# Kernel optimization log

Hardware: AMD Instinct MI355X
Metric: run time of the kernel (lower is better)

The kernel has to match this reference:

```python
import jax, jax.numpy as jnp
import numpy as np

B, N = 16, 300000          # batch, total anchors per image (all FPN levels concatenated)
PRE, POST = 2000, 1000     # num_pre_nms, num_post_nms
NMS_THR = 0.7
MIN_SIZE = 1e-3            # proposal_min_size
IMG_H, IMG_W = 800.0, 1333.0


def setup_inputs() -> dict:
    key = jax.random.key(0)
    k1, k2, k3, k4, k5, k6 = jax.random.split(key, 6)
    cls = jax.random.normal(k1, (B, N), dtype=jnp.float32)
    reg = jax.random.normal(k2, (B, N, 4), dtype=jnp.float32) * 0.1
    # anchors as valid (cx,cy,w,h)->(x1,y1,x2,y2) boxes inside the image
    cx = jax.random.uniform(k3, (B, N), dtype=jnp.float32, minval=0.0, maxval=IMG_W)
    cy = jax.random.uniform(k4, (B, N), dtype=jnp.float32, minval=0.0, maxval=IMG_H)
    w = jax.random.uniform(k5, (B, N), dtype=jnp.float32, minval=16.0, maxval=256.0)
    h = jax.random.uniform(k6, (B, N), dtype=jnp.float32, minval=16.0, maxval=256.0)
    anchors = jnp.stack([cx - 0.5 * w, cy - 0.5 * h, cx + 0.5 * w, cy + 0.5 * h], axis=-1)
    return {"cls": cls, "reg": reg, "anchors": anchors}


def _decode(anchor, reg):
    aw = anchor[:, 2] - anchor[:, 0]
    ah = anchor[:, 3] - anchor[:, 1]
    acx = anchor[:, 0] + 0.5 * aw
    acy = anchor[:, 1] + 0.5 * ah
    dx, dy, dw, dh = reg[:, 0], reg[:, 1], reg[:, 2], reg[:, 3]
    pcx = dx * aw + acx
    pcy = dy * ah + acy
    pw = jnp.exp(dw) * aw
    ph = jnp.exp(dh) * ah
    return jnp.stack([pcx - 0.5 * pw, pcy - 0.5 * ph, pcx + 0.5 * pw, pcy + 0.5 * ph], axis=-1)


def _iou_matrix(boxes):
    # boxes: [K,4] -> pairwise IoU [K,K]
    area = (boxes[:, 2] - boxes[:, 0]) * (boxes[:, 3] - boxes[:, 1])
    lt = jnp.maximum(boxes[:, None, :2], boxes[None, :, :2])
    rb = jnp.minimum(boxes[:, None, 2:], boxes[None, :, 2:])
    wh = jnp.clip(rb - lt, 0.0)
    inter = wh[..., 0] * wh[..., 1]
    union = area[:, None] + area[None, :] - inter
    return inter / jnp.maximum(union, 1e-8)


def _per_image(score, reg, anchor):
    # topk pre-NMS selection (lax.top_k returns score-descending order)
    top_s, idx = jax.lax.top_k(score, PRE)
    boxes = _decode(anchor[idx], reg[idx].reshape(-1, 4))
    # clip to image bounds
    bounds = jnp.array([IMG_W, IMG_H, IMG_W, IMG_H], dtype=boxes.dtype)
    boxes = jnp.clip(boxes, 0.0, bounds)
    # remove small boxes (mask instead of dynamic removal)
    w = boxes[:, 2] - boxes[:, 0]
    h = boxes[:, 3] - boxes[:, 1]
    valid = (w >= MIN_SIZE) & (h >= MIN_SIZE)
    s = jnp.where(valid, top_s, -jnp.inf)
    order = jnp.argsort(-s)  # score-descending, invalid last
    boxes = boxes[order]
    valid = valid[order]
    # greedy NMS: iterate highest-score-first, suppress later boxes with IoU > thr
    iou = _iou_matrix(boxes)
    rng = jnp.arange(PRE)
    def body(i, keep):
        sup = (iou[i] > NMS_THR) & keep[i]
        return keep & jnp.logical_not(sup & (rng > i))
    keep = jax.lax.fori_loop(0, PRE, body, valid)
    # gather kept boxes (score order preserved), pad with zeros past count
    sel = jnp.argsort(jnp.logical_not(keep), stable=True)[:POST]
    return boxes[sel] * keep[sel][:, None].astype(boxes.dtype)


def reference(cls, reg, anchors):
    # [B, POST, 4] proposals per image (zero-padded where fewer than POST kept)
    return jax.vmap(_per_image)(cls, reg, anchors)
```

## Files before the change

kernel.cpp:

```cpp
#include <hip/hip_runtime.h>

#define NB 16
#define NN 300000
#define PRE 2000
#define POST 1000

typedef unsigned long long ull;

static const size_t OFF_HIST1   = 0;
static const size_t OFF_HIST2   = 65536;
static const size_t OFF_HIST3   = 196608;
static const size_t OFF_CANDCNT = 327680;
static const size_t OFF_EQCNT   = 327936;
static const size_t OFF_BITMAP  = 328192;
static const size_t OFF_B1      = 332288;
static const size_t OFF_NEED1   = 332544;
static const size_t OFF_B2      = 332800;
static const size_t OFF_NEED2   = 333056;
static const size_t OFF_B3      = 333312;
static const size_t OFF_NEED3   = 333568;
static const size_t ZERO_BYTES  = 333824;
static const size_t OFF_CAND    = 333824;
static const size_t OFF_EQBUF   = 464896;
static const size_t OFF_SORTED  = 989184;
static const size_t OFF_NVALID  = 1501184;
static const size_t OFF_MASK    = 1501440;

__device__ __forceinline__ unsigned f2u(float f){
  unsigned b = __float_as_uint(f);
  return (b & 0x80000000u) ? ~b : (b | 0x80000000u);
}

#define H1REP 8
#define H1STRIDE 1025
__global__ void k_hist1(const float* __restrict__ cls, unsigned* __restrict__ hist){
  __shared__ unsigned h[H1REP * H1STRIDE];
  int img = blockIdx.y;
  for (int i = threadIdx.x; i < H1REP * H1STRIDE; i += blockDim.x) h[i] = 0;
  __syncthreads();
  const float* p = cls + (size_t)img * NN;
  int stride = gridDim.x * blockDim.x;
  unsigned rep = (threadIdx.x & (H1REP - 1)) * H1STRIDE;
  for (int i = blockIdx.x * blockDim.x + threadIdx.x; i < NN; i += stride)
    atomicAdd(&h[rep + (f2u(p[i]) >> 22)], 1u);
  __syncthreads();
  unsigned* g = hist + img * 1024;
  for (int i = threadIdx.x; i < 1024; i += blockDim.x){
    unsigned v = 0;
    for (int r = 0; r < H1REP; r++) v += h[r * H1STRIDE + i];
    if (v) atomicAdd(&g[i], v);
  }
}

__global__ void k_scan(const unsigned* __restrict__ hist, int bins,
                       const unsigned* __restrict__ tgt, unsigned K0,
                       unsigned* __restrict__ outBin, unsigned* __restrict__ outNeed){
  int img = blockIdx.x;
  int t = threadIdx.x;
  const unsigned* hh = hist + img * bins;
  unsigned K = tgt ? tgt[img] : K0;
  int per = bins >> 8;
  unsigned s = 0;
  for (int q = 0; q < per; q++) s += hh[bins - 1 - (t * per + q)];
  __shared__ unsigned arr[256];
  arr[t] = s;
  __syncthreads();
  for (int off = 1; off < 256; off <<= 1){
    unsigned v = (t >= off) ? arr[t - off] : 0u;
    __syncthreads();
    arr[t] += v;
    __syncthreads();
  }
  unsigned incl = arr[t], excl = incl - s;
  if (excl < K && K <= incl){
    unsigned c = excl;
    for (int q = 0; q < per; q++){
      int b = bins - 1 - (t * per + q);
      unsigned cnt = hh[b];
      if (c + cnt >= K){ outBin[img] = (unsigned)b; outNeed[img] = K - c; break; }
      c += cnt;
    }
  }
}

__global__ void k_hist2(const float* __restrict__ cls, const unsigned* __restrict__ b1,
                        unsigned* __restrict__ hist){
  int img = blockIdx.y;
  unsigned bb1 = b1[img];
  const float* p = cls + (size_t)img * NN;
  unsigned* g = hist + img * 2048;
  int stride = gridDim.x * blockDim.x;
  for (int i = blockIdx.x * blockDim.x + threadIdx.x; i < NN; i += stride){
    unsigned u = f2u(p[i]);
    if ((u >> 22) == bb1) atomicAdd(&g[(u >> 11) & 0x7FFu], 1u);
  }
}

__global__ void k_hist3(const float* __restrict__ cls, const unsigned* __restrict__ b1,
                        const unsigned* __restrict__ b2, unsigned* __restrict__ hist){
  int img = blockIdx.y;
  unsigned pref = (b1[img] << 11) | b2[img];
  const float* p = cls + (size_t)img * NN;
  unsigned* g = hist + img * 2048;
  int stride = gridDim.x * blockDim.x;
  for (int i = blockIdx.x * blockDim.x + threadIdx.x; i < NN; i += stride){
    unsigned u = f2u(p[i]);
    if ((u >> 11) == pref) atomicAdd(&g[u & 0x7FFu], 1u);
  }
}

__global__ void k_compact(const float* __restrict__ cls, const unsigned* __restrict__ b1,
                          const unsigned* __restrict__ b2, const unsigned* __restrict__ b3,
                          unsigned* __restrict__ cand, unsigned* __restrict__ candCnt,
                          unsigned* __restrict__ eqbuf, unsigned* __restrict__ eqCnt){
  __shared__ unsigned lc[1024];
  __shared__ unsigned le[256];
  __shared__ unsigned lcn, len_, baseC, baseE;
  int img = blockIdx.y;
  if (threadIdx.x == 0){ lcn = 0; len_ = 0; }
  __syncthreads();
  unsigned T = (b1[img] << 22) | (b2[img] << 11) | b3[img];
  const float* p = cls + (size_t)img * NN;
  int stride = gridDim.x * blockDim.x;
  for (int i = blockIdx.x * blockDim.x + threadIdx.x; i < NN; i += stride){
    unsigned u = f2u(p[i]);
    if (u > T){
      unsigned pos = atomicAdd(&lcn, 1u);
      if (pos < 1024u) lc[pos] = (unsigned)i;
      else { unsigned g = atomicAdd(&candCnt[img], 1u); if (g < 2048u) cand[img * 2048 + g] = (unsigned)i; }
    } else if (u == T){
      unsigned pos = atomicAdd(&len_, 1u);
      if (pos < 256u) le[pos] = (unsigned)i;
      else { unsigned g = atomicAdd(&eqCnt[img], 1u); if (g < 8192u) eqbuf[img * 8192 + g] = (unsigned)i; }
    }
  }
  __syncthreads();
  unsigned nc = lcn < 1024u ? lcn : 1024u;
  unsigned ne = len_ < 256u ? len_ : 256u;
  if (threadIdx.x == 0){
    if (nc) baseC = atomicAdd(&candCnt[img], nc);
    if (ne) baseE = atomicAdd(&eqCnt[img], ne);
  }
  __syncthreads();
  for (unsigned t = threadIdx.x; t < nc; t += blockDim.x){
    unsigned g = baseC + t;
    if (g < 2048u) cand[img * 2048 + g] = lc[t];
  }
  for (unsigned t = threadIdx.x; t < ne; t += blockDim.x){
    unsigned g = baseE + t;
    if (g < 8192u) eqbuf[img * 8192 + g] = le[t];
  }
}

__global__ __launch_bounds__(1024) void k_sortd(
    const float* __restrict__ cls, const float* __restrict__ reg,
    const float* __restrict__ anch,
    const unsigned* __restrict__ cand, const unsigned* __restrict__ candCnt,
    const unsigned* __restrict__ eqbuf, const unsigned* __restrict__ eqCnt,
    const unsigned* __restrict__ need3,
    float* __restrict__ sorted, unsigned* __restrict__ nvalid){
  __shared__ ull k[2048];
  __shared__ unsigned short p[2048];
  __shared__ unsigned cidx[2048];
  __shared__ float4 bxs[2048];
  __shared__ unsigned nv;
  int img = blockIdx.x, tid = threadIdx.x;
  unsigned need = need3[img];
  unsigned ec = eqCnt[img]; if (ec > 8192u) ec = 8192u;
  unsigned base = candCnt[img]; if (base > 2048u) base = 2048u;
  const unsigned* eq = eqbuf + img * 8192;
  for (int t = tid; t < 2048; t += 1024)
    cidx[t] = (t < (int)base) ? cand[img * 2048 + t] : 0xFFFFFFFFu;
  if (tid == 0) nv = 0;
  __syncthreads();
  if (need >= ec){
    for (unsigned t = tid; t < ec; t += 1024){
      unsigned g = base + t; if (g < 2048u) cidx[g] = eq[t];
    }
  } else {
    for (unsigned t = tid; t < ec; t += 1024){
      unsigned v = eq[t], r = 0;
      for (unsigned s = 0; s < ec; s++) r += (eq[s] < v) ? 1u : 0u;
      if (r < need && base + r < 2048u) cidx[base + r] = v;
    }
  }
  __syncthreads();
  for (int t = tid; t < 2048; t += 1024){
    unsigned i = cidx[t];
    ull key = 0ull;
    float4 box = make_float4(0.f, 0.f, 0.f, 0.f);
    if (t < PRE && i < NN){
      size_t gi = (size_t)img * NN + i;
      float4 a = ((const float4*)anch)[gi];
      float4 r4 = ((const float4*)reg)[gi];
      float sc = cls[gi];
      float aw = a.z - a.x, ah = a.w - a.y;
      float acx = a.x + 0.5f * aw, acy = a.y + 0.5f * ah;
      float pcx = r4.x * aw + acx, pcy = r4.y * ah + acy;
      float pw = expf(r4.z) * aw, ph = expf(r4.w) * ah;
      float x1 = pcx - 0.5f * pw, y1 = pcy - 0.5f * ph;
      float x2 = pcx + 0.5f * pw, y2 = pcy + 0.5f * ph;
      x1 = fminf(fmaxf(x1, 0.f), 1333.f); x2 = fminf(fmaxf(x2, 0.f), 1333.f);
      y1 = fminf(fmaxf(y1, 0.f), 800.f);  y2 = fminf(fmaxf(y2, 0.f), 800.f);
      bool valid = ((x2 - x1) >= 0.001f) && ((y2 - y1) >= 0.001f);
      unsigned up = valid ? f2u(sc) : 0u;
      key = ((ull)up << 32) | (ull)(0xFFFFFFFFu - i);
      box = make_float4(x1, y1, x2, y2);
    }
    k[t] = key; bxs[t] = box; p[t] = (unsigned short)t;
  }
  __syncthreads();
  for (int kk = 2; kk <= 2048; kk <<= 1){
    for (int j = kk >> 1; j > 0; j >>= 1){
      for (int i = tid; i < 2048; i += 1024){
        int ixj = i ^ j;
        if (ixj > i){
          ull ka = k[i], kb = k[ixj];
          bool up = ((i & kk) == 0);
          if (up ? (ka < kb) : (ka > kb)){
            k[i] = kb; k[ixj] = ka;
            unsigned short t2 = p[i]; p[i] = p[ixj]; p[ixj] = t2;
          }
        }
      }
      __syncthreads();
    }
  }
  unsigned c = 0;
  for (int r = tid; r < PRE; r += 1024){
    ((float4*)sorted)[img * PRE + r] = bxs[p[r]];
    if ((unsigned)(k[r] >> 32) != 0u) c++;
  }
  atomicAdd(&nv, c);
  __syncthreads();
  if (tid == 0) nvalid[img] = nv;
}

__global__ __launch_bounds__(512) void k_mask(const float* __restrict__ sorted,
                                              const unsigned* __restrict__ nvalid,
                                              ull* __restrict__ mask, ull* __restrict__ bitmap){
  __shared__ float4 bx[PRE];
  __shared__ float  ar[PRE];
  __shared__ unsigned rowflag[16];
  int img = blockIdx.y, tid = threadIdx.x;
  if (tid < 16) rowflag[tid] = 0;
  for (int i = tid; i < PRE; i += 512){
    float4 b = ((const float4*)sorted)[img * PRE + i];
    bx[i] = b;
    ar[i] = (b.z - b.x) * (b.w - b.y);
  }
  __syncthreads();
  int row = blockIdx.x * 16 + (tid >> 5);
  int w = tid & 31;
  float4 bi = bx[row];
  float ai = ar[row];
  int qlo = (row >= w) ? (((row - w) >> 5) + 1) : 0;
  int qhi = ((PRE - 1 - w) >> 5) + 1;
  ull m = 0;
  for (int q = qlo; q < qhi; q++){
    int j = (q << 5) + w;
    float4 bj = bx[j];
    float xx1 = fmaxf(bi.x, bj.x), yy1 = fmaxf(bi.y, bj.y);
    float xx2 = fminf(bi.z, bj.z), yy2 = fminf(bi.w, bj.w);
    float ww = fmaxf(xx2 - xx1, 0.f), hh = fmaxf(yy2 - yy1, 0.f);
    float inter = ww * hh;
    float uni = ai + ar[j] - inter;
    if (inter / fmaxf(uni, 1e-8f) > 0.7f) m |= (1ull << q);
  }
  mask[((size_t)(img * PRE + row)) * 32 + w] = m;
  if (m) atomicOr(&rowflag[tid >> 5], 1u);
  __syncthreads();
  if (tid < 16){
    int r = blockIdx.x * 16 + tid;
    if (rowflag[tid] && r < (int)nvalid[img])
      atomicOr(&bitmap[img * 32 + (r >> 6)], 1ull << (r & 63));
  }
}

__global__ __launch_bounds__(256) void k_nms(const ull* __restrict__ mask,
                                             const ull* __restrict__ bitmap,
                                             const unsigned* __restrict__ nvalid,
                                             const float* __restrict__ sorted,
                                             float* __restrict__ out){
  __shared__ unsigned rows[2048];
  __shared__ int mcount;
  __shared__ ull cache[192 * 32];
  __shared__ ull keepP[32];
  __shared__ ull keepLin[32];
  __shared__ unsigned cntArr[32], preArr[32];
  int img = blockIdx.x, tid = threadIdx.x;
  int lane = tid & 63, wave = tid >> 6;
  if (tid == 0){
    int m = 0;
    for (int w0 = 0; w0 < 32; w0++){
      ull bits = bitmap[img * 32 + w0];
      while (bits){
        int b = __ffsll(bits) - 1;
        rows[m++] = (unsigned)(w0 * 64 + b);
        bits &= bits - 1;
      }
    }
    mcount = m;
  }
  __syncthreads();
  int m = mcount;
  ull remv = 0;
  for (int base = 0; base < m; base += 192){
    int cnt = min(192, m - base);
    for (int t = tid; t < cnt * 32; t += 256){
      unsigned rr = rows[base + (t >> 5)];
      cache[t] = mask[((size_t)(img * PRE + rr)) * 32 + (t & 31)];
    }
    __syncthreads();
    if (wave == 0){
      for (int q = 0; q < cnt; q++){
        int i = (int)rows[base + q];
        int wi = i & 31, bi = i >> 5;
        int sup = (lane == wi) && ((remv >> bi) & 1ull);
        if (!__any(sup)){
          if (lane < 32) remv |= cache[(q << 5) + lane];
        }
      }
    }
    __syncthreads();
  }
  int nv = (int)nvalid[img];
  if (wave == 0 && lane < 32){
    int cnt2 = (nv > lane) ? (((nv - 1 - lane) >> 5) + 1) : 0;
    ull vm = (cnt2 >= 64) ? ~0ull : ((1ull << cnt2) - 1ull);
    keepP[lane] = (~remv) & vm;
  }
  __syncthreads();
  if (tid < 32){
    ull lin = 0;
    for (int kk = 0; kk < 64; kk++)
      lin |= ((keepP[kk & 31] >> (2 * tid + (kk >> 5))) & 1ull) << kk;
    keepLin[tid] = lin;
    cntArr[tid] = (unsigned)__popcll(lin);
  }
  __syncthreads();
  if (tid < 32){
    unsigned pre = 0;
    for (int w0 = 0; w0 < tid; w0++) pre += cntArr[w0];
    preArr[tid] = pre;
  }
  __syncthreads();
  for (int i = tid; i < PRE; i += 256){
    int w0 = i >> 6, b = i & 63;
    ull kw = keepLin[w0];
    if ((kw >> b) & 1ull){
      unsigned rank = preArr[w0] + (unsigned)__popcll(kw & ((1ull << b) - 1ull));
      if (rank < POST)
        ((float4*)out)[img * POST + rank] = ((const float4*)sorted)[img * PRE + i];
    }
  }
}

extern "C" void kernel_launch(void* const* d_in, const int* in_sizes, int n_in,
                              void* d_out, int out_size, void* d_ws, size_t ws_size,
                              hipStream_t stream){
  const float* cls  = (const float*)d_in[0];
  const float* reg  = (const float*)d_in[1];
  const float* anch = (const float*)d_in[2];
  float* out = (float*)d_out;
  char* ws = (char*)d_ws;

  unsigned* hist1   = (unsigned*)(ws + OFF_HIST1);
  unsigned* hist2   = (unsigned*)(ws + OFF_HIST2);
  unsigned* hist3   = (unsigned*)(ws + OFF_HIST3);
  unsigned* candCnt = (unsigned*)(ws + OFF_CANDCNT);
  unsigned* eqCnt   = (unsigned*)(ws + OFF_EQCNT);
  ull*      bitmap  = (ull*)     (ws + OFF_BITMAP);
  unsigned* b1      = (unsigned*)(ws + OFF_B1);
  unsigned* need1   = (unsigned*)(ws + OFF_NEED1);
  unsigned* b2      = (unsigned*)(ws + OFF_B2);
  unsigned* need2   = (unsigned*)(ws + OFF_NEED2);
  unsigned* b3      = (unsigned*)(ws + OFF_B3);
  unsigned* need3   = (unsigned*)(ws + OFF_NEED3);
  unsigned* cand    = (unsigned*)(ws + OFF_CAND);
  unsigned* eqbuf   = (unsigned*)(ws + OFF_EQBUF);
  float*    sorted  = (float*)   (ws + OFF_SORTED);
  unsigned* nvalid  = (unsigned*)(ws + OFF_NVALID);
  ull*      mask    = (ull*)     (ws + OFF_MASK);

  hipMemsetAsync(ws, 0, ZERO_BYTES, stream);
  hipMemsetAsync(d_out, 0, (size_t)out_size * sizeof(float), stream);

  k_hist1<<<dim3(64, NB), 256, 0, stream>>>(cls, hist1);
  k_scan <<<NB, 256, 0, stream>>>(hist1, 1024, (const unsigned*)nullptr, 2000u, b1, need1);
  k_hist2<<<dim3(64, NB), 256, 0, stream>>>(cls, b1, hist2);
  k_scan <<<NB, 256, 0, stream>>>(hist2, 2048, need1, 0u, b2, need2);
  k_hist3<<<dim3(64, NB), 256, 0, stream>>>(cls, b1, b2, hist3);
  k_scan <<<NB, 256, 0, stream>>>(hist3, 2048, need2, 0u, b3, need3);
  k_compact<<<dim3(64, NB), 256, 0, stream>>>(cls, b1, b2, b3, cand, candCnt, eqbuf, eqCnt);
  k_sortd<<<NB, 1024, 0, stream>>>(cls, reg, anch, cand, candCnt, eqbuf, eqCnt, need3,
                                   sorted, nvalid);
  k_mask<<<dim3(PRE / 16, NB), 512, 0, stream>>>(sorted, nvalid, mask, bitmap);
  k_nms<<<NB, 256, 0, stream>>>(mask, bitmap, nvalid, sorted, out);
}
```

Baseline: 352.1 us.

## Split per-image sort into finalize, parallel decode, and rank-based scatter kernels

Replaces the single-block-per-image kernel that decoded boxes and ran a shared-memory bitonic sort with three kernels. A small finalize kernel completes the candidate list, a grid-wide decode kernel writes keys and boxes to global scratch and counts valid boxes with ballot plus atomics, and a rank kernel spread over 8 blocks per image computes each element's position by counting larger keys. This spreads the sort work across many more compute units and removes the long chain of barrier-separated bitonic stages. The cost is two extra launches, global round trips for keys and boxes, and quadratic comparison work per image.

```diff
diff --git a/kernel.cpp b/kernel.cpp
--- a/kernel.cpp
+++ b/kernel.cpp
@@ -19,12 +19,14 @@
 static const size_t OFF_NEED2   = 333056;
 static const size_t OFF_B3      = 333312;
 static const size_t OFF_NEED3   = 333568;
-static const size_t ZERO_BYTES  = 333824;
-static const size_t OFF_CAND    = 333824;
-static const size_t OFF_EQBUF   = 464896;
-static const size_t OFF_SORTED  = 989184;
-static const size_t OFF_NVALID  = 1501184;
-static const size_t OFF_MASK    = 1501440;
+static const size_t OFF_NVALID  = 333824;
+static const size_t ZERO_BYTES  = 334080;
+static const size_t OFF_CAND    = 334080;
+static const size_t OFF_EQBUF   = 465152;
+static const size_t OFF_KEYS    = 989440;
+static const size_t OFF_BOXTMP  = 1251584;
+static const size_t OFF_SORTED  = 1775872;
+static const size_t OFF_MASK    = 2287872;
 
 __device__ __forceinline__ unsigned f2u(float f){
   unsigned b = __float_as_uint(f);
@@ -152,52 +154,47 @@
   }
 }
 
-__global__ __launch_bounds__(1024) void k_sortd(
-    const float* __restrict__ cls, const float* __restrict__ reg,
-    const float* __restrict__ anch,
-    const unsigned* __restrict__ cand, const unsigned* __restrict__ candCnt,
-    const unsigned* __restrict__ eqbuf, const unsigned* __restrict__ eqCnt,
-    const unsigned* __restrict__ need3,
-    float* __restrict__ sorted, unsigned* __restrict__ nvalid){
-  __shared__ ull k[2048];
-  __shared__ unsigned short p[2048];
-  __shared__ unsigned cidx[2048];
-  __shared__ float4 bxs[2048];
-  __shared__ unsigned nv;
+__global__ void k_finalize(unsigned* __restrict__ cand, const unsigned* __restrict__ candCnt,
+                           const unsigned* __restrict__ eqbuf, const unsigned* __restrict__ eqCnt,
+                           const unsigned* __restrict__ need3){
   int img = blockIdx.x, tid = threadIdx.x;
   unsigned need = need3[img];
   unsigned ec = eqCnt[img]; if (ec > 8192u) ec = 8192u;
-  unsigned base = candCnt[img]; if (base > 2048u) base = 2048u;
+  unsigned base = candCnt[img];
   const unsigned* eq = eqbuf + img * 8192;
-  for (int t = tid; t < 2048; t += 1024)
-    cidx[t] = (t < (int)base) ? cand[img * 2048 + t] : 0xFFFFFFFFu;
-  if (tid == 0) nv = 0;
-  __syncthreads();
+  unsigned* c = cand + img * 2048;
   if (need >= ec){
-    for (unsigned t = tid; t < ec; t += 1024){
-      unsigned g = base + t; if (g < 2048u) cidx[g] = eq[t];
-    }
-  } else {
-    for (unsigned t = tid; t < ec; t += 1024){
-      unsigned v = eq[t], r = 0;
-      for (unsigned s = 0; s < ec; s++) r += (eq[s] < v) ? 1u : 0u;
-      if (r < need && base + r < 2048u) cidx[base + r] = v;
-    }
-  }
-  __syncthreads();
-  for (int t = tid; t < 2048; t += 1024){
-    unsigned i = cidx[t];
-    ull key = 0ull;
-    float4 box = make_float4(0.f, 0.f, 0.f, 0.f);
-    if (t < PRE && i < NN){
+    for (unsigned t = tid; t < ec; t += 256) if (base + t < 2048u) c[base + t] = eq[t];
+    return;
+  }
+  for (unsigned t = tid; t < ec; t += 256){
+    unsigned v = eq[t], r = 0;
+    for (unsigned s = 0; s < ec; s++) r += (eq[s] < v) ? 1u : 0u;
+    if (r < need && base + r < 2048u) c[base + r] = v;
+  }
+}
+
+__global__ void k_decode(const float* __restrict__ cls, const float* __restrict__ reg,
+                         const float* __restrict__ anch, const unsigned* __restrict__ cand,
+                         float* __restrict__ boxTmp, ull* __restrict__ keys,
+                         unsigned* __restrict__ nvalid){
+  int s = blockIdx.x * blockDim.x + threadIdx.x;
+  if (s >= NB * 2048) return;
+  int img = s >> 11, slot = s & 2047;
+  ull key = 0ull;
+  float4 box = make_float4(0.f, 0.f, 0.f, 0.f);
+  bool counted = false;
+  if (slot < PRE){
+    unsigned i = cand[img * 2048 + slot];
+    if (i < NN){
       size_t gi = (size_t)img * NN + i;
       float4 a = ((const float4*)anch)[gi];
-      float4 r4 = ((const float4*)reg)[gi];
+      float4 r = ((const float4*)reg)[gi];
       float sc = cls[gi];
       float aw = a.z - a.x, ah = a.w - a.y;
       float acx = a.x + 0.5f * aw, acy = a.y + 0.5f * ah;
-      float pcx = r4.x * aw + acx, pcy = r4.y * ah + acy;
-      float pw = expf(r4.z) * aw, ph = expf(r4.w) * ah;
+      float pcx = r.x * aw + acx, pcy = r.y * ah + acy;
+      float pw = expf(r.z) * aw, ph = expf(r.w) * ah;
       float x1 = pcx - 0.5f * pw, y1 = pcy - 0.5f * ph;
       float x2 = pcx + 0.5f * pw, y2 = pcy + 0.5f * ph;
       x1 = fminf(fmaxf(x1, 0.f), 1333.f); x2 = fminf(fmaxf(x2, 0.f), 1333.f);
@@ -206,34 +203,30 @@
       unsigned up = valid ? f2u(sc) : 0u;
       key = ((ull)up << 32) | (ull)(0xFFFFFFFFu - i);
       box = make_float4(x1, y1, x2, y2);
-    }
-    k[t] = key; bxs[t] = box; p[t] = (unsigned short)t;
-  }
-  __syncthreads();
-  for (int kk = 2; kk <= 2048; kk <<= 1){
-    for (int j = kk >> 1; j > 0; j >>= 1){
-      for (int i = tid; i < 2048; i += 1024){
-        int ixj = i ^ j;
-        if (ixj > i){
-          ull ka = k[i], kb = k[ixj];
-          bool up = ((i & kk) == 0);
-          if (up ? (ka < kb) : (ka > kb)){
-            k[i] = kb; k[ixj] = ka;
-            unsigned short t2 = p[i]; p[i] = p[ixj]; p[ixj] = t2;
-          }
-        }
-      }
-      __syncthreads();
-    }
-  }
-  unsigned c = 0;
-  for (int r = tid; r < PRE; r += 1024){
-    ((float4*)sorted)[img * PRE + r] = bxs[p[r]];
-    if ((unsigned)(k[r] >> 32) != 0u) c++;
-  }
-  atomicAdd(&nv, c);
-  __syncthreads();
-  if (tid == 0) nvalid[img] = nv;
+      counted = valid;
+    }
+  }
+  keys[img * 2048 + slot] = key;
+  ((float4*)boxTmp)[img * 2048 + slot] = box;
+  ull bal = __ballot(counted);
+  if ((threadIdx.x & 63) == 0 && bal)
+    atomicAdd(&nvalid[img], (unsigned)__popcll(bal));
+}
+
+__global__ __launch_bounds__(256) void k_rank(const ull* __restrict__ keys,
+                                              const float* __restrict__ boxTmp,
+                                              float* __restrict__ sorted){
+  __shared__ ull lk[2048];
+  int img = blockIdx.y;
+  int e = blockIdx.x * 256 + threadIdx.x;
+  for (int t = threadIdx.x; t < 2048; t += 256) lk[t] = keys[img * 2048 + t];
+  __syncthreads();
+  ull me = lk[e];
+  unsigned rank = 0;
+  #pragma unroll 8
+  for (int j = 0; j < 2048; j++) rank += (lk[j] > me) ? 1u : 0u;
+  if (rank < PRE)
+    ((float4*)sorted)[img * PRE + rank] = ((const float4*)boxTmp)[img * 2048 + e];
 }
 
 __global__ __launch_bounds__(512) void k_mask(const float* __restrict__ sorted,
@@ -377,10 +370,12 @@
   unsigned* need2   = (unsigned*)(ws + OFF_NEED2);
   unsigned* b3      = (unsigned*)(ws + OFF_B3);
   unsigned* need3   = (unsigned*)(ws + OFF_NEED3);
+  unsigned* nvalid  = (unsigned*)(ws + OFF_NVALID);
   unsigned* cand    = (unsigned*)(ws + OFF_CAND);
   unsigned* eqbuf   = (unsigned*)(ws + OFF_EQBUF);
+  ull*      keys    = (ull*)     (ws + OFF_KEYS);
+  float*    boxTmp  = (float*)   (ws + OFF_BOXTMP);
   float*    sorted  = (float*)   (ws + OFF_SORTED);
-  unsigned* nvalid  = (unsigned*)(ws + OFF_NVALID);
   ull*      mask    = (ull*)     (ws + OFF_MASK);
 
   hipMemsetAsync(ws, 0, ZERO_BYTES, stream);
@@ -393,8 +388,9 @@
   k_hist3<<<dim3(64, NB), 256, 0, stream>>>(cls, b1, b2, hist3);
   k_scan <<<NB, 256, 0, stream>>>(hist3, 2048, need2, 0u, b3, need3);
   k_compact<<<dim3(64, NB), 256, 0, stream>>>(cls, b1, b2, b3, cand, candCnt, eqbuf, eqCnt);
-  k_sortd<<<NB, 1024, 0, stream>>>(cls, reg, anch, cand, candCnt, eqbuf, eqCnt, need3,
-                                   sorted, nvalid);
+  k_finalize<<<NB, 256, 0, stream>>>(cand, candCnt, eqbuf, eqCnt, need3);
+  k_decode<<<(NB * 2048) / 256, 256, 0, stream>>>(cls, reg, anch, cand, boxTmp, keys, nvalid);
+  k_rank<<<dim3(8, NB), 256, 0, stream>>>(keys, boxTmp, sorted);
   k_mask<<<dim3(PRE / 16, NB), 512, 0, stream>>>(sorted, nvalid, mask, bitmap);
   k_nms<<<NB, 256, 0, stream>>>(mask, bitmap, nvalid, sorted, out);
 }
```

New measurement: 336.0 us. 4.6% less time.
